# Performance work log

Hardware: AMD Instinct MI355X
Metric: run time of the kernel (lower is better)

Reference implementation:

```python
import jax, jax.numpy as jnp
import numpy as np

EPS = 1e-12  # torch F.normalize eps

def l2_normalize(x):
    n = jnp.sqrt(jnp.sum(x * x, axis=-1, keepdims=True))
    return x / jnp.maximum(n, EPS)

def entmax15(z):
    # Exact 1.5-entmax (Peters & Martins 2019), rowwise over last dim.
    z = z / 2.0
    z_srt = jnp.flip(jnp.sort(z, axis=-1), axis=-1)  # descending
    k = jnp.arange(1, z.shape[-1] + 1, dtype=z.dtype)
    mean = jnp.cumsum(z_srt, axis=-1) / k
    mean_sq = jnp.cumsum(z_srt * z_srt, axis=-1) / k
    ss = k * (mean_sq - mean * mean)
    delta = jnp.clip((1.0 - ss) / k, 0.0, None)
    tau = mean - jnp.sqrt(delta)
    support = (tau <= z_srt).astype(jnp.int32)
    k_star = jnp.sum(support, axis=-1, keepdims=True)  # support size >= 1
    tau_star = jnp.take_along_axis(tau, k_star - 1, axis=-1)
    p = jnp.clip(z - tau_star, 0.0, None)
    return p * p

def setup_inputs() -> dict:
    key = jax.random.key(0)
    ks = jax.random.split(key, 4)
    E, S, H, P = 8192, 8192, 512, 64
    lim = float(np.sqrt(6.0 / (H + P)))  # xavier_uniform bound
    return {
        "edge_repr": jax.random.normal(ks[0], (E, H), dtype=jnp.float32),
        "sub_repr": jax.random.normal(ks[1], (S, H), dtype=jnp.float32),
        "W_sub": jax.random.uniform(ks[2], (P, H), jnp.float32, -lim, lim),
        "b_sub": jnp.zeros((P,), jnp.float32),
        "W_edge": jax.random.uniform(ks[3], (P, H), jnp.float32, -lim, lim),
        "b_edge": jnp.zeros((P,), jnp.float32),
        "log_scale": jnp.asarray(np.log(5.0), jnp.float32),
    }

def reference(edge_repr, sub_repr, W_sub, b_sub, W_edge, b_edge, log_scale):
    sub_proj = l2_normalize(sub_repr @ W_sub.T + b_sub)    # [S, P]
    edge_proj = l2_normalize(edge_repr @ W_edge.T + b_edge)  # [E, P]
    scale = jnp.clip(jnp.exp(log_scale), 0.5, 20.0)
    scores = (sub_proj @ edge_proj.T) * scale  # [S, E]
    return entmax15(scores)
```

## Files before the change

kernel.cpp:

```cpp
#include <hip/hip_runtime.h>
#include <math.h>

#define NEWTON_ITERS 14

__global__ __launch_bounds__(256) void proj_norm_kernel(
    const float* __restrict__ Xsub, const float* __restrict__ Xedge,
    const float* __restrict__ Wsub, const float* __restrict__ bsub,
    const float* __restrict__ Wedge, const float* __restrict__ bedge,
    float* __restrict__ Psub, float* __restrict__ Pedge)
{
    const int mat = blockIdx.y;
    const float* X  = mat ? Xedge : Xsub;
    const float* W  = mat ? Wedge : Wsub;
    const float* Bv = mat ? bedge : bsub;
    float* OUT      = mat ? Pedge : Psub;

    const int r0 = blockIdx.x * 64;
    const int t  = threadIdx.x;
    const int lr = t & 63;
    const int q  = t >> 6;
    const int c0 = q * 16;

    __shared__ float4 xs[64 * 33];
    __shared__ float4 wq[64 * 33];
    __shared__ float  red[4][64];

    float acc[16];
#pragma unroll
    for (int i = 0; i < 16; ++i) acc[i] = 0.0f;

    for (int ch = 0; ch < 4; ++ch) {
        const int kb = ch * 128;
#pragma unroll
        for (int i = 0; i < 8; ++i) {
            int e = t + 256 * i;
            int row = e >> 5, kc = e & 31;
            xs[row * 33 + kc] = *(const float4*)(X + (size_t)(r0 + row) * 512 + kb + kc * 4);
            wq[row * 33 + kc] = *(const float4*)(W + (size_t)row * 512 + kb + kc * 4);
        }
        __syncthreads();
#pragma unroll 4
        for (int kc = 0; kc < 32; ++kc) {
            const float4 x4 = xs[lr * 33 + kc];
#pragma unroll
            for (int cc = 0; cc < 16; ++cc) {
                const float4 w4 = wq[(c0 + cc) * 33 + kc];
                acc[cc] = fmaf(x4.x, w4.x, acc[cc]);
                acc[cc] = fmaf(x4.y, w4.y, acc[cc]);
                acc[cc] = fmaf(x4.z, w4.z, acc[cc]);
                acc[cc] = fmaf(x4.w, w4.w, acc[cc]);
            }
        }
        __syncthreads();
    }

    float ss = 0.0f;
#pragma unroll
    for (int cc = 0; cc < 16; ++cc) {
        acc[cc] += Bv[c0 + cc];
        ss = fmaf(acc[cc], acc[cc], ss);
    }
    red[q][lr] = ss;
    __syncthreads();
    const float tot = red[0][lr] + red[1][lr] + red[2][lr] + red[3][lr];
    const float inv = 1.0f / fmaxf(sqrtf(tot), 1e-12f);

    float* op = OUT + (size_t)(r0 + lr) * 64 + c0;
#pragma unroll
    for (int v = 0; v < 4; ++v) {
        float4 o;
        o.x = acc[v * 4 + 0] * inv;
        o.y = acc[v * 4 + 1] * inv;
        o.z = acc[v * 4 + 2] * inv;
        o.w = acc[v * 4 + 3] * inv;
        *(float4*)(op + v * 4) = o;
    }
}

__global__ __launch_bounds__(256) void scores_kernel(
    const float* __restrict__ Psub, const float* __restrict__ Pedge,
    const float* __restrict__ log_scale, float* __restrict__ Z)
{
    __shared__ float la[64 * 132];
    __shared__ float lb[64 * 132];
    const int t  = threadIdx.x;
    const int m0 = blockIdx.y * 128;
    const int n0 = blockIdx.x * 128;

#pragma unroll
    for (int i = 0; i < 8; ++i) {
        int e = t + 256 * i;
        int m = e & 127, kq = e >> 7;
        float4 va = *(const float4*)(Psub + (size_t)(m0 + m) * 64 + kq * 4);
        la[(kq * 4 + 0) * 132 + m] = va.x;
        la[(kq * 4 + 1) * 132 + m] = va.y;
        la[(kq * 4 + 2) * 132 + m] = va.z;
        la[(kq * 4 + 3) * 132 + m] = va.w;
        float4 vb = *(const float4*)(Pedge + (size_t)(n0 + m) * 64 + kq * 4);
        lb[(kq * 4 + 0) * 132 + m] = vb.x;
        lb[(kq * 4 + 1) * 132 + m] = vb.y;
        lb[(kq * 4 + 2) * 132 + m] = vb.z;
        lb[(kq * 4 + 3) * 132 + m] = vb.w;
    }
    __syncthreads();

    const int tx = t & 15, ty = t >> 4;
    float acc[8][8] = {};

#pragma unroll 8
    for (int k = 0; k < 64; ++k) {
        const float4 a0 = *(const float4*)&la[k * 132 + ty * 4];
        const float4 a1 = *(const float4*)&la[k * 132 + ty * 4 + 64];
        const float4 b0 = *(const float4*)&lb[k * 132 + tx * 4];
        const float4 b1 = *(const float4*)&lb[k * 132 + tx * 4 + 64];
        const float av[8] = {a0.x, a0.y, a0.z, a0.w, a1.x, a1.y, a1.z, a1.w};
        const float bv[8] = {b0.x, b0.y, b0.z, b0.w, b1.x, b1.y, b1.z, b1.w};
#pragma unroll
        for (int i = 0; i < 8; ++i)
#pragma unroll
            for (int j = 0; j < 8; ++j)
                acc[i][j] = fmaf(av[i], bv[j], acc[i][j]);
    }

    float sc = expf(log_scale[0]);
    sc = fminf(fmaxf(sc, 0.5f), 20.0f);
    const float zs = sc * 0.5f;

#pragma unroll
    for (int i = 0; i < 8; ++i) {
        const int rl = (i < 4) ? (ty * 4 + i) : (64 + ty * 4 + (i - 4));
        float* rp = Z + (size_t)(m0 + rl) * 8192 + n0;
        float4 o0, o1;
        o0.x = acc[i][0] * zs; o0.y = acc[i][1] * zs;
        o0.z = acc[i][2] * zs; o0.w = acc[i][3] * zs;
        o1.x = acc[i][4] * zs; o1.y = acc[i][5] * zs;
        o1.z = acc[i][6] * zs; o1.w = acc[i][7] * zs;
        *(float4*)(rp + tx * 4)      = o0;
        *(float4*)(rp + tx * 4 + 64) = o1;
    }
}

__global__ __launch_bounds__(256) void entmax_kernel(float* __restrict__ Z)
{
    const int row = blockIdx.x;
    const int t   = threadIdx.x;
    float* rp = Z + (size_t)row * 8192;

    float4 v[8];
#pragma unroll
    for (int j = 0; j < 8; ++j)
        v[j] = *(const float4*)(rp + t * 4 + 1024 * j);

    float m = -1e30f;
#pragma unroll
    for (int j = 0; j < 8; ++j)
        m = fmaxf(m, fmaxf(fmaxf(v[j].x, v[j].y), fmaxf(v[j].z, v[j].w)));
#pragma unroll
    for (int off = 32; off; off >>= 1)
        m = fmaxf(m, __shfl_xor(m, off, 64));

    __shared__ float rmax[4];
    __shared__ float rf[NEWTON_ITERS][4];
    __shared__ float rg[NEWTON_ITERS][4];
    const int wid = t >> 6;
    if ((t & 63) == 0) rmax[wid] = m;
    __syncthreads();
    m = fmaxf(fmaxf(rmax[0], rmax[1]), fmaxf(rmax[2], rmax[3]));

    float tau = m - 1.0f;

    for (int it = 0; it < NEWTON_ITERS; ++it) {
        float f = 0.0f, g = 0.0f;
#pragma unroll
        for (int j = 0; j < 8; ++j) {
            float d;
            d = fmaxf(v[j].x - tau, 0.0f); f = fmaf(d, d, f); g += d;
            d = fmaxf(v[j].y - tau, 0.0f); f = fmaf(d, d, f); g += d;
            d = fmaxf(v[j].z - tau, 0.0f); f = fmaf(d, d, f); g += d;
            d = fmaxf(v[j].w - tau, 0.0f); f = fmaf(d, d, f); g += d;
        }
#pragma unroll
        for (int off = 32; off; off >>= 1) {
            f += __shfl_xor(f, off, 64);
            g += __shfl_xor(g, off, 64);
        }
        if ((t & 63) == 0) { rf[it][wid] = f; rg[it][wid] = g; }
        __syncthreads();
        f = rf[it][0] + rf[it][1] + rf[it][2] + rf[it][3];
        g = rg[it][0] + rg[it][1] + rg[it][2] + rg[it][3];
        tau += (f - 1.0f) / (2.0f * g);
    }

#pragma unroll
    for (int j = 0; j < 8; ++j) {
        float4 o; float d;
        d = fmaxf(v[j].x - tau, 0.0f); o.x = d * d;
        d = fmaxf(v[j].y - tau, 0.0f); o.y = d * d;
        d = fmaxf(v[j].z - tau, 0.0f); o.z = d * d;
        d = fmaxf(v[j].w - tau, 0.0f); o.w = d * d;
        *(float4*)(rp + t * 4 + 1024 * j) = o;
    }
}

extern "C" void kernel_launch(void* const* d_in, const int* in_sizes, int n_in,
                              void* d_out, int out_size, void* d_ws, size_t ws_size,
                              hipStream_t stream)
{
    const float* edge_repr = (const float*)d_in[0];
    const float* sub_repr  = (const float*)d_in[1];
    const float* W_sub     = (const float*)d_in[2];
    const float* b_sub     = (const float*)d_in[3];
    const float* W_edge    = (const float*)d_in[4];
    const float* b_edge    = (const float*)d_in[5];
    const float* log_scale = (const float*)d_in[6];
    float* out = (float*)d_out;

    float* sub_proj  = (float*)d_ws;
    float* edge_proj = (float*)d_ws + (size_t)8192 * 64;

    proj_norm_kernel<<<dim3(128, 2), 256, 0, stream>>>(
        sub_repr, edge_repr, W_sub, b_sub, W_edge, b_edge, sub_proj, edge_proj);

    scores_kernel<<<dim3(64, 64), 256, 0, stream>>>(
        sub_proj, edge_proj, log_scale, out);

    entmax_kernel<<<8192, 256, 0, stream>>>(out);
}
```

Measured before the change: 509.8 us.

## Fuse score GEMM with entmax in registers and store edge projections transposed

The score matmul and the entmax bisection/Newton pass are merged into one kernel. Each 1024-thread block computes 8 full rows of scores in registers and runs the tau iterations on them directly, so the 256MB score matrix is no longer written and then read back before the final write. The projection kernel is retiled to 4x4 per thread and writes the edge projection transposed so the fused kernel can stream coalesced B columns. Waves whose values all sit below tau skip the per-iteration reduction work. In exchange, each block rereads the whole transposed edge matrix from L2, and the per-thread register footprint is large.

```diff
diff --git a/kernel.cpp b/kernel.cpp
--- a/kernel.cpp
+++ b/kernel.cpp
@@ -1,204 +1,262 @@
 #include <hip/hip_runtime.h>
 #include <math.h>
 
-#define NEWTON_ITERS 14
+#define ITERS 14
 
 __global__ __launch_bounds__(256) void proj_norm_kernel(
     const float* __restrict__ Xsub, const float* __restrict__ Xedge,
     const float* __restrict__ Wsub, const float* __restrict__ bsub,
     const float* __restrict__ Wedge, const float* __restrict__ bedge,
-    float* __restrict__ Psub, float* __restrict__ Pedge)
+    float* __restrict__ subP, float* __restrict__ edgeT)
 {
     const int mat = blockIdx.y;
     const float* X  = mat ? Xedge : Xsub;
     const float* W  = mat ? Wedge : Wsub;
     const float* Bv = mat ? bedge : bsub;
-    float* OUT      = mat ? Pedge : Psub;
 
     const int r0 = blockIdx.x * 64;
     const int t  = threadIdx.x;
-    const int lr = t & 63;
-    const int q  = t >> 6;
-    const int c0 = q * 16;
-
-    __shared__ float4 xs[64 * 33];
-    __shared__ float4 wq[64 * 33];
-    __shared__ float  red[4][64];
-
-    float acc[16];
-#pragma unroll
-    for (int i = 0; i < 16; ++i) acc[i] = 0.0f;
-
-    for (int ch = 0; ch < 4; ++ch) {
-        const int kb = ch * 128;
-#pragma unroll
-        for (int i = 0; i < 8; ++i) {
+    const int tx = t & 15, ty = t >> 4;
+
+    __shared__ float xs[64 * 68];
+    __shared__ float ws[64 * 68];
+    __shared__ float tr[64 * 68];
+
+    float acc[4][4] = {};
+
+    for (int ch = 0; ch < 8; ++ch) {
+        const int kb = ch * 64;
+#pragma unroll
+        for (int i = 0; i < 4; ++i) {
             int e = t + 256 * i;
-            int row = e >> 5, kc = e & 31;
-            xs[row * 33 + kc] = *(const float4*)(X + (size_t)(r0 + row) * 512 + kb + kc * 4);
-            wq[row * 33 + kc] = *(const float4*)(W + (size_t)row * 512 + kb + kc * 4);
-        }
-        __syncthreads();
-#pragma unroll 4
-        for (int kc = 0; kc < 32; ++kc) {
-            const float4 x4 = xs[lr * 33 + kc];
-#pragma unroll
-            for (int cc = 0; cc < 16; ++cc) {
-                const float4 w4 = wq[(c0 + cc) * 33 + kc];
-                acc[cc] = fmaf(x4.x, w4.x, acc[cc]);
-                acc[cc] = fmaf(x4.y, w4.y, acc[cc]);
-                acc[cc] = fmaf(x4.z, w4.z, acc[cc]);
-                acc[cc] = fmaf(x4.w, w4.w, acc[cc]);
-            }
-        }
-        __syncthreads();
-    }
-
-    float ss = 0.0f;
-#pragma unroll
-    for (int cc = 0; cc < 16; ++cc) {
-        acc[cc] += Bv[c0 + cc];
-        ss = fmaf(acc[cc], acc[cc], ss);
-    }
-    red[q][lr] = ss;
+            int row = e & 63, kq = e >> 6;
+            float4 xv = *(const float4*)(X + (size_t)(r0 + row) * 512 + kb + kq * 4);
+            xs[(kq * 4 + 0) * 68 + row] = xv.x;
+            xs[(kq * 4 + 1) * 68 + row] = xv.y;
+            xs[(kq * 4 + 2) * 68 + row] = xv.z;
+            xs[(kq * 4 + 3) * 68 + row] = xv.w;
+            float4 wv = *(const float4*)(W + (size_t)row * 512 + kb + kq * 4);
+            ws[(kq * 4 + 0) * 68 + row] = wv.x;
+            ws[(kq * 4 + 1) * 68 + row] = wv.y;
+            ws[(kq * 4 + 2) * 68 + row] = wv.z;
+            ws[(kq * 4 + 3) * 68 + row] = wv.w;
+        }
+        __syncthreads();
+#pragma unroll 8
+        for (int k = 0; k < 64; ++k) {
+            const float4 a4 = *(const float4*)&xs[k * 68 + ty * 4];
+            const float4 b4 = *(const float4*)&ws[k * 68 + tx * 4];
+            const float av[4] = {a4.x, a4.y, a4.z, a4.w};
+#pragma unroll
+            for (int i = 0; i < 4; ++i) {
+                acc[i][0] = fmaf(av[i], b4.x, acc[i][0]);
+                acc[i][1] = fmaf(av[i], b4.y, acc[i][1]);
+                acc[i][2] = fmaf(av[i], b4.z, acc[i][2]);
+                acc[i][3] = fmaf(av[i], b4.w, acc[i][3]);
+            }
+        }
+        __syncthreads();
+    }
+
+    const float4 bb = *(const float4*)(Bv + tx * 4);
+    float ss[4];
+#pragma unroll
+    for (int i = 0; i < 4; ++i) {
+        acc[i][0] += bb.x; acc[i][1] += bb.y; acc[i][2] += bb.z; acc[i][3] += bb.w;
+        float s = acc[i][0]*acc[i][0] + acc[i][1]*acc[i][1]
+                + acc[i][2]*acc[i][2] + acc[i][3]*acc[i][3];
+#pragma unroll
+        for (int off = 1; off <= 8; off <<= 1)
+            s += __shfl_xor(s, off, 64);
+        ss[i] = s;
+    }
+
+    if (mat == 0) {
+#pragma unroll
+        for (int i = 0; i < 4; ++i) {
+            const float inv = 1.0f / fmaxf(sqrtf(ss[i]), 1e-12f);
+            float4 o;
+            o.x = acc[i][0]*inv; o.y = acc[i][1]*inv; o.z = acc[i][2]*inv; o.w = acc[i][3]*inv;
+            *(float4*)(subP + (size_t)(r0 + ty * 4 + i) * 64 + tx * 4) = o;
+        }
+    } else {
+        __syncthreads();
+#pragma unroll
+        for (int i = 0; i < 4; ++i) {
+            const float inv = 1.0f / fmaxf(sqrtf(ss[i]), 1e-12f);
+#pragma unroll
+            for (int j = 0; j < 4; ++j)
+                tr[(tx * 4 + j) * 68 + ty * 4 + i] = acc[i][j] * inv;
+        }
+        __syncthreads();
+#pragma unroll
+        for (int i = 0; i < 4; ++i) {
+            int e = t + 256 * i;
+            int c = e >> 4, rq = e & 15;
+            *(float4*)(edgeT + (size_t)c * 8192 + r0 + rq * 4) =
+                *(const float4*)&tr[c * 68 + rq * 4];
+        }
+    }
+}
+
+#define FMA4(ACC, S, B) \
+    ACC.x = fmaf(S, B.x, ACC.x); ACC.y = fmaf(S, B.y, ACC.y); \
+    ACC.z = fmaf(S, B.z, ACC.z); ACC.w = fmaf(S, B.w, ACC.w);
+
+__global__ __launch_bounds__(1024, 4) void fused_score_entmax_kernel(
+    const float* __restrict__ subP, const float* __restrict__ edgeT,
+    const float* __restrict__ log_scale, float* __restrict__ out)
+{
+    const int t    = threadIdx.x;
+    const int lane = t & 63;
+    const int wid  = t >> 6;
+    const int r0   = blockIdx.x * 8;
+    const int c0   = t * 4;
+
+    __shared__ float asT[64 * 8];
+    __shared__ float tbl[16 * 16];
+    __shared__ float tauL[8];
+
+    if (t < 512) {
+        int r = t >> 6, k = t & 63;
+        asT[k * 8 + r] = subP[(size_t)(r0 + r) * 64 + k];
+    }
     __syncthreads();
-    const float tot = red[0][lr] + red[1][lr] + red[2][lr] + red[3][lr];
-    const float inv = 1.0f / fmaxf(sqrtf(tot), 1e-12f);
-
-    float* op = OUT + (size_t)(r0 + lr) * 64 + c0;
-#pragma unroll
-    for (int v = 0; v < 4; ++v) {
-        float4 o;
-        o.x = acc[v * 4 + 0] * inv;
-        o.y = acc[v * 4 + 1] * inv;
-        o.z = acc[v * 4 + 2] * inv;
-        o.w = acc[v * 4 + 3] * inv;
-        *(float4*)(op + v * 4) = o;
-    }
-}
-
-__global__ __launch_bounds__(256) void scores_kernel(
-    const float* __restrict__ Psub, const float* __restrict__ Pedge,
-    const float* __restrict__ log_scale, float* __restrict__ Z)
-{
-    __shared__ float la[64 * 132];
-    __shared__ float lb[64 * 132];
-    const int t  = threadIdx.x;
-    const int m0 = blockIdx.y * 128;
-    const int n0 = blockIdx.x * 128;
-
-#pragma unroll
-    for (int i = 0; i < 8; ++i) {
-        int e = t + 256 * i;
-        int m = e & 127, kq = e >> 7;
-        float4 va = *(const float4*)(Psub + (size_t)(m0 + m) * 64 + kq * 4);
-        la[(kq * 4 + 0) * 132 + m] = va.x;
-        la[(kq * 4 + 1) * 132 + m] = va.y;
-        la[(kq * 4 + 2) * 132 + m] = va.z;
-        la[(kq * 4 + 3) * 132 + m] = va.w;
-        float4 vb = *(const float4*)(Pedge + (size_t)(n0 + m) * 64 + kq * 4);
-        lb[(kq * 4 + 0) * 132 + m] = vb.x;
-        lb[(kq * 4 + 1) * 132 + m] = vb.y;
-        lb[(kq * 4 + 2) * 132 + m] = vb.z;
-        lb[(kq * 4 + 3) * 132 + m] = vb.w;
-    }
-    __syncthreads();
-
-    const int tx = t & 15, ty = t >> 4;
-    float acc[8][8] = {};
-
-#pragma unroll 8
+
+    float4 acc0[8], acc1[8];
+#pragma unroll
+    for (int r = 0; r < 8; ++r) {
+        acc0[r] = make_float4(0.f, 0.f, 0.f, 0.f);
+        acc1[r] = make_float4(0.f, 0.f, 0.f, 0.f);
+    }
+
+#pragma unroll 2
     for (int k = 0; k < 64; ++k) {
-        const float4 a0 = *(const float4*)&la[k * 132 + ty * 4];
-        const float4 a1 = *(const float4*)&la[k * 132 + ty * 4 + 64];
-        const float4 b0 = *(const float4*)&lb[k * 132 + tx * 4];
-        const float4 b1 = *(const float4*)&lb[k * 132 + tx * 4 + 64];
-        const float av[8] = {a0.x, a0.y, a0.z, a0.w, a1.x, a1.y, a1.z, a1.w};
-        const float bv[8] = {b0.x, b0.y, b0.z, b0.w, b1.x, b1.y, b1.z, b1.w};
-#pragma unroll
-        for (int i = 0; i < 8; ++i)
-#pragma unroll
-            for (int j = 0; j < 8; ++j)
-                acc[i][j] = fmaf(av[i], bv[j], acc[i][j]);
+        const float4 b0 = *(const float4*)(edgeT + (size_t)k * 8192 + c0);
+        const float4 b1 = *(const float4*)(edgeT + (size_t)k * 8192 + c0 + 4096);
+        const float4 a0 = *(const float4*)&asT[k * 8];
+        const float4 a1 = *(const float4*)&asT[k * 8 + 4];
+        FMA4(acc0[0], a0.x, b0); FMA4(acc1[0], a0.x, b1);
+        FMA4(acc0[1], a0.y, b0); FMA4(acc1[1], a0.y, b1);
+        FMA4(acc0[2], a0.z, b0); FMA4(acc1[2], a0.z, b1);
+        FMA4(acc0[3], a0.w, b0); FMA4(acc1[3], a0.w, b1);
+        FMA4(acc0[4], a1.x, b0); FMA4(acc1[4], a1.x, b1);
+        FMA4(acc0[5], a1.y, b0); FMA4(acc1[5], a1.y, b1);
+        FMA4(acc0[6], a1.z, b0); FMA4(acc1[6], a1.z, b1);
+        FMA4(acc0[7], a1.w, b0); FMA4(acc1[7], a1.w, b1);
     }
 
     float sc = expf(log_scale[0]);
     sc = fminf(fmaxf(sc, 0.5f), 20.0f);
     const float zs = sc * 0.5f;
-
-#pragma unroll
-    for (int i = 0; i < 8; ++i) {
-        const int rl = (i < 4) ? (ty * 4 + i) : (64 + ty * 4 + (i - 4));
-        float* rp = Z + (size_t)(m0 + rl) * 8192 + n0;
-        float4 o0, o1;
-        o0.x = acc[i][0] * zs; o0.y = acc[i][1] * zs;
-        o0.z = acc[i][2] * zs; o0.w = acc[i][3] * zs;
-        o1.x = acc[i][4] * zs; o1.y = acc[i][5] * zs;
-        o1.z = acc[i][6] * zs; o1.w = acc[i][7] * zs;
-        *(float4*)(rp + tx * 4)      = o0;
-        *(float4*)(rp + tx * 4 + 64) = o1;
-    }
-}
-
-__global__ __launch_bounds__(256) void entmax_kernel(float* __restrict__ Z)
-{
-    const int row = blockIdx.x;
-    const int t   = threadIdx.x;
-    float* rp = Z + (size_t)row * 8192;
-
-    float4 v[8];
-#pragma unroll
-    for (int j = 0; j < 8; ++j)
-        v[j] = *(const float4*)(rp + t * 4 + 1024 * j);
-
-    float m = -1e30f;
-#pragma unroll
-    for (int j = 0; j < 8; ++j)
-        m = fmaxf(m, fmaxf(fmaxf(v[j].x, v[j].y), fmaxf(v[j].z, v[j].w)));
-#pragma unroll
-    for (int off = 32; off; off >>= 1)
-        m = fmaxf(m, __shfl_xor(m, off, 64));
-
-    __shared__ float rmax[4];
-    __shared__ float rf[NEWTON_ITERS][4];
-    __shared__ float rg[NEWTON_ITERS][4];
-    const int wid = t >> 6;
-    if ((t & 63) == 0) rmax[wid] = m;
+#pragma unroll
+    for (int r = 0; r < 8; ++r) {
+        acc0[r].x *= zs; acc0[r].y *= zs; acc0[r].z *= zs; acc0[r].w *= zs;
+        acc1[r].x *= zs; acc1[r].y *= zs; acc1[r].z *= zs; acc1[r].w *= zs;
+    }
+
+    float wlm[8];
+#pragma unroll
+    for (int r = 0; r < 8; ++r) {
+        float m = fmaxf(fmaxf(fmaxf(acc0[r].x, acc0[r].y), fmaxf(acc0[r].z, acc0[r].w)),
+                        fmaxf(fmaxf(acc1[r].x, acc1[r].y), fmaxf(acc1[r].z, acc1[r].w)));
+#pragma unroll
+        for (int off = 32; off; off >>= 1)
+            m = fmaxf(m, __shfl_xor(m, off, 64));
+        wlm[r] = m;
+    }
+    if (lane == 0) {
+#pragma unroll
+        for (int r = 0; r < 8; ++r) tbl[wid * 16 + r] = wlm[r];
+    }
     __syncthreads();
-    m = fmaxf(fmaxf(rmax[0], rmax[1]), fmaxf(rmax[2], rmax[3]));
-
-    float tau = m - 1.0f;
-
-    for (int it = 0; it < NEWTON_ITERS; ++it) {
-        float f = 0.0f, g = 0.0f;
-#pragma unroll
-        for (int j = 0; j < 8; ++j) {
-            float d;
-            d = fmaxf(v[j].x - tau, 0.0f); f = fmaf(d, d, f); g += d;
-            d = fmaxf(v[j].y - tau, 0.0f); f = fmaf(d, d, f); g += d;
-            d = fmaxf(v[j].z - tau, 0.0f); f = fmaf(d, d, f); g += d;
-            d = fmaxf(v[j].w - tau, 0.0f); f = fmaf(d, d, f); g += d;
-        }
-#pragma unroll
-        for (int off = 32; off; off >>= 1) {
-            f += __shfl_xor(f, off, 64);
-            g += __shfl_xor(g, off, 64);
-        }
-        if ((t & 63) == 0) { rf[it][wid] = f; rg[it][wid] = g; }
-        __syncthreads();
-        f = rf[it][0] + rf[it][1] + rf[it][2] + rf[it][3];
-        g = rg[it][0] + rg[it][1] + rg[it][2] + rg[it][3];
-        tau += (f - 1.0f) / (2.0f * g);
-    }
-
-#pragma unroll
-    for (int j = 0; j < 8; ++j) {
-        float4 o; float d;
-        d = fmaxf(v[j].x - tau, 0.0f); o.x = d * d;
-        d = fmaxf(v[j].y - tau, 0.0f); o.y = d * d;
-        d = fmaxf(v[j].z - tau, 0.0f); o.z = d * d;
-        d = fmaxf(v[j].w - tau, 0.0f); o.w = d * d;
-        *(float4*)(rp + t * 4 + 1024 * j) = o;
+    if (t < 8) {
+        float m = -1e30f;
+#pragma unroll
+        for (int w = 0; w < 16; ++w) m = fmaxf(m, tbl[w * 16 + t]);
+        tauL[t] = m - 1.0f;
+    }
+    __syncthreads();
+
+    float tau[8];
+    {
+        const float4 tA = *(const float4*)&tauL[0];
+        const float4 tB = *(const float4*)&tauL[4];
+        tau[0]=tA.x; tau[1]=tA.y; tau[2]=tA.z; tau[3]=tA.w;
+        tau[4]=tB.x; tau[5]=tB.y; tau[6]=tB.z; tau[7]=tB.w;
+    }
+
+    for (int it = 0; it < ITERS; ++it) {
+        bool active = false;
+#pragma unroll
+        for (int r = 0; r < 8; ++r) active |= (wlm[r] > tau[r]);
+        if (active) {
+            float fv[8], gv[8];
+#pragma unroll
+            for (int r = 0; r < 8; ++r) {
+                float f = 0.f, g = 0.f, d;
+                d = fmaxf(acc0[r].x - tau[r], 0.f); f = fmaf(d, d, f); g += d;
+                d = fmaxf(acc0[r].y - tau[r], 0.f); f = fmaf(d, d, f); g += d;
+                d = fmaxf(acc0[r].z - tau[r], 0.f); f = fmaf(d, d, f); g += d;
+                d = fmaxf(acc0[r].w - tau[r], 0.f); f = fmaf(d, d, f); g += d;
+                d = fmaxf(acc1[r].x - tau[r], 0.f); f = fmaf(d, d, f); g += d;
+                d = fmaxf(acc1[r].y - tau[r], 0.f); f = fmaf(d, d, f); g += d;
+                d = fmaxf(acc1[r].z - tau[r], 0.f); f = fmaf(d, d, f); g += d;
+                d = fmaxf(acc1[r].w - tau[r], 0.f); f = fmaf(d, d, f); g += d;
+                fv[r] = f; gv[r] = g;
+            }
+#pragma unroll
+            for (int off = 32; off; off >>= 1) {
+#pragma unroll
+                for (int r = 0; r < 8; ++r) {
+                    fv[r] += __shfl_xor(fv[r], off, 64);
+                    gv[r] += __shfl_xor(gv[r], off, 64);
+                }
+            }
+            if (lane == 0) {
+#pragma unroll
+                for (int r = 0; r < 8; ++r) {
+                    tbl[wid * 16 + r]     = fv[r];
+                    tbl[wid * 16 + 8 + r] = gv[r];
+                }
+            }
+        } else if (lane == 0) {
+#pragma unroll
+            for (int i = 0; i < 16; ++i) tbl[wid * 16 + i] = 0.f;
+        }
+        __syncthreads();
+        if (t < 8) {
+            float F = 0.f, G = 0.f;
+#pragma unroll
+            for (int w = 0; w < 16; ++w) {
+                F += tbl[w * 16 + t];
+                G += tbl[w * 16 + 8 + t];
+            }
+            tauL[t] += (F - 1.0f) / (2.0f * G);
+        }
+        __syncthreads();
+        {
+            const float4 tA = *(const float4*)&tauL[0];
+            const float4 tB = *(const float4*)&tauL[4];
+            tau[0]=tA.x; tau[1]=tA.y; tau[2]=tA.z; tau[3]=tA.w;
+            tau[4]=tB.x; tau[5]=tB.y; tau[6]=tB.z; tau[7]=tB.w;
+        }
+    }
+
+#pragma unroll
+    for (int r = 0; r < 8; ++r) {
+        float* op = out + (size_t)(r0 + r) * 8192;
+        float4 p0, p1; float d;
+        d = fmaxf(acc0[r].x - tau[r], 0.f); p0.x = d * d;
+        d = fmaxf(acc0[r].y - tau[r], 0.f); p0.y = d * d;
+        d = fmaxf(acc0[r].z - tau[r], 0.f); p0.z = d * d;
+        d = fmaxf(acc0[r].w - tau[r], 0.f); p0.w = d * d;
+        d = fmaxf(acc1[r].x - tau[r], 0.f); p1.x = d * d;
+        d = fmaxf(acc1[r].y - tau[r], 0.f); p1.y = d * d;
+        d = fmaxf(acc1[r].z - tau[r], 0.f); p1.z = d * d;
+        d = fmaxf(acc1[r].w - tau[r], 0.f); p1.w = d * d;
+        *(float4*)(op + c0)        = p0;
+        *(float4*)(op + c0 + 4096) = p1;
     }
 }
 
@@ -215,14 +273,12 @@
     const float* log_scale = (const float*)d_in[6];
     float* out = (float*)d_out;
 
-    float* sub_proj  = (float*)d_ws;
-    float* edge_proj = (float*)d_ws + (size_t)8192 * 64;
+    float* sub_proj = (float*)d_ws;
+    float* edgeT    = (float*)d_ws + (size_t)8192 * 64;
 
     proj_norm_kernel<<<dim3(128, 2), 256, 0, stream>>>(
-        sub_repr, edge_repr, W_sub, b_sub, W_edge, b_edge, sub_proj, edge_proj);
-
-    scores_kernel<<<dim3(64, 64), 256, 0, stream>>>(
-        sub_proj, edge_proj, log_scale, out);
-
-    entmax_kernel<<<8192, 256, 0, stream>>>(out);
+        sub_repr, edge_repr, W_sub, b_sub, W_edge, b_edge, sub_proj, edgeT);
+
+    fused_score_entmax_kernel<<<1024, 1024, 0, stream>>>(
+        sub_proj, edgeT, log_scale, out);
 }
```

After: 786.1 us. +54.2%, slower.
